# Performance work log

Measured on AMD Instinct MI355X. Metric: run time of the kernel, lower is better.

## Reference

```python
import jax, jax.numpy as jnp
import numpy as np

N_NODES = 10000
N_GRAPHS = 64
IN_DIM = 256
HID = 256
N_CLASSES = 10
N_EDGES = 320000


def _gcn_conv(x, W, b, src, dst):
    # PyG GCNConv: h = x @ W; add self-loops (weight 1); symmetric norm D^-1/2 (A+I) D^-1/2; aggregate; + b
    N = x.shape[0]
    h = x @ W  # [N, H]
    loops = jnp.arange(N, dtype=src.dtype)
    s = jnp.concatenate([src, loops])
    d = jnp.concatenate([dst, loops])
    w = jnp.ones(s.shape[0], dtype=x.dtype)
    deg = jax.ops.segment_sum(w, d, num_segments=N)
    dinv = jnp.where(deg > 0, jax.lax.rsqrt(jnp.maximum(deg, 1.0)), 0.0)
    norm = dinv[s] * dinv[d]  # [E+N]
    msg = h[s] * norm[:, None]  # gather + scale
    out = jax.ops.segment_sum(msg, d, num_segments=N)  # scatter-add
    return out + b


def setup_inputs() -> dict:
    key = jax.random.key(0)
    ks = jax.random.split(key, 12)
    x = jax.random.normal(ks[0], (N_NODES, IN_DIM), dtype=jnp.float32)
    edge_index = jax.random.randint(ks[1], (2, N_EDGES), 0, N_NODES, dtype=jnp.int64)
    batch = jnp.sort(jax.random.randint(ks[2], (N_NODES,), 0, N_GRAPHS, dtype=jnp.int64))
    g = 1.0 / np.sqrt(IN_DIM)
    W1 = jax.random.uniform(ks[3], (IN_DIM, HID), jnp.float32, -g, g)
    b1 = jnp.zeros((HID,), jnp.float32)
    gh = 1.0 / np.sqrt(HID)
    W2 = jax.random.uniform(ks[4], (HID, HID), jnp.float32, -gh, gh)
    b2 = jnp.zeros((HID,), jnp.float32)
    W3 = jax.random.uniform(ks[5], (HID, HID), jnp.float32, -gh, gh)
    b3 = jnp.zeros((HID,), jnp.float32)
    Wlin = jax.random.uniform(ks[6], (HID, N_CLASSES), jnp.float32, -gh, gh)
    blin = jax.random.uniform(ks[7], (N_CLASSES,), jnp.float32, -gh, gh)
    return {"x": x, "W1": W1, "b1": b1, "W2": W2, "b2": b2, "W3": W3, "b3": b3,
            "Wlin": Wlin, "blin": blin, "edge_index": edge_index, "batch": batch}


def reference(x, W1, b1, W2, b2, W3, b3, Wlin, blin, edge_index, batch):
    src, dst = edge_index[0], edge_index[1]
    h = jax.nn.relu(_gcn_conv(x, W1, b1, src, dst))
    h = jax.nn.relu(_gcn_conv(h, W2, b2, src, dst))
    h = jax.nn.relu(_gcn_conv(h, W3, b3, src, dst))
    # global mean pool over graphs (dropout is identity in eval mode)
    sums = jax.ops.segment_sum(h, batch, num_segments=N_GRAPHS)  # [G, H]
    cnts = jax.ops.segment_sum(jnp.ones((h.shape[0],), h.dtype), batch, num_segments=N_GRAPHS)
    pooled = sums / jnp.maximum(cnts, 1.0)[:, None]
    logits = pooled @ Wlin + blin
    return jax.nn.log_softmax(logits, axis=-1)
```

## Files before the change

kernel.cpp:

```cpp
#include <hip/hip_runtime.h>
#include <hip/hip_bf16.h>
#include <math.h>

#define HIDDEN 256
#define NCLS 10

typedef __attribute__((ext_vector_type(8))) short short8;
typedef __attribute__((ext_vector_type(4))) float f32x4;

static __device__ __forceinline__ float bf16lo(unsigned u) {
    return __uint_as_float((u & 0xffffu) << 16);
}
static __device__ __forceinline__ float bf16hi(unsigned u) {
    return __uint_as_float(u & 0xffff0000u);
}
static __device__ __forceinline__ unsigned short f2bf(float f) {
    unsigned x = __float_as_uint(f);
    x += 0x7fffu + ((x >> 16) & 1u);
    return (unsigned short)(x >> 16);
}
static __device__ __forceinline__ unsigned pack2(float lo, float hi) {
    return (unsigned)f2bf(lo) | ((unsigned)f2bf(hi) << 16);
}

static __device__ __forceinline__ void fma8(float* acc, uint4 u, float w) {
    acc[0] = fmaf(bf16lo(u.x), w, acc[0]);
    acc[1] = fmaf(bf16hi(u.x), w, acc[1]);
    acc[2] = fmaf(bf16lo(u.y), w, acc[2]);
    acc[3] = fmaf(bf16hi(u.y), w, acc[3]);
    acc[4] = fmaf(bf16lo(u.z), w, acc[4]);
    acc[5] = fmaf(bf16hi(u.z), w, acc[5]);
    acc[6] = fmaf(bf16lo(u.w), w, acc[6]);
    acc[7] = fmaf(bf16hi(u.w), w, acc[7]);
}

__global__ void k_init(int* ecnt, int* cursor, int N) {
    int i = blockIdx.x * blockDim.x + threadIdx.x;
    if (i < N) { ecnt[i] = 0; cursor[i] = 0; }
}

__global__ void k_count(const int* __restrict__ dst, int* __restrict__ ecnt, int E) {
    int e = blockIdx.x * blockDim.x + threadIdx.x;
    if (e < E) atomicAdd(&ecnt[dst[e]], 1);
}

__global__ void k_dinv(const int* __restrict__ ecnt, float* __restrict__ dinv, int N) {
    int i = blockIdx.x * blockDim.x + threadIdx.x;
    if (i < N) dinv[i] = rsqrtf((float)(ecnt[i] + 1));
}

__global__ void k_scan(const int* __restrict__ ecnt, int* __restrict__ rowstart, int N, int E) {
    __shared__ int sums[1024];
    int t = threadIdx.x;
    const int CH = (N + 1023) / 1024;
    int base = t * CH;
    int local = 0;
    for (int i = 0; i < CH; ++i) {
        int idx = base + i;
        if (idx < N) local += ecnt[idx];
    }
    sums[t] = local;
    __syncthreads();
    for (int off = 1; off < 1024; off <<= 1) {
        int v = (t >= off) ? sums[t - off] : 0;
        __syncthreads();
        sums[t] += v;
        __syncthreads();
    }
    int run = (t == 0) ? 0 : sums[t - 1];
    for (int i = 0; i < CH; ++i) {
        int idx = base + i;
        if (idx < N) { rowstart[idx] = run; run += ecnt[idx]; }
    }
    if (t == 0) rowstart[N] = E;
}

__global__ void k_fill(const int* __restrict__ src, const int* __restrict__ dst,
                       const float* __restrict__ dinv,
                       const int* __restrict__ rowstart, int* __restrict__ cursor,
                       uint2* __restrict__ csr, int E) {
    int e = blockIdx.x * blockDim.x + threadIdx.x;
    if (e < E) {
        int d = dst[e];
        int s = src[e];
        int pos = rowstart[d] + atomicAdd(&cursor[d], 1);
        uint2 ent;
        ent.x = (unsigned)s;
        ent.y = __float_as_uint(dinv[s] * dinv[d]);
        csr[pos] = ent;
    }
}

__global__ void k_cvt(const float* __restrict__ in, unsigned* __restrict__ out, int n4) {
    int i = blockIdx.x * blockDim.x + threadIdx.x;
    if (i < n4) {
        float4 v = reinterpret_cast<const float4*>(in)[i];
        uint2 o;
        o.x = pack2(v.x, v.y);
        o.y = pack2(v.z, v.w);
        reinterpret_cast<uint2*>(out)[i] = o;
    }
}

__global__ void k_packW(const float* __restrict__ W, short8* __restrict__ P) {
    int id = blockIdx.x * blockDim.x + threadIdx.x;
    int l = id & 63;
    int t = (id >> 6) & 15;
    int s = id >> 10;
    int col = t * 16 + (l & 15);
    int k0 = s * 32 + (l >> 4) * 8;
    short8 v;
#pragma unroll
    for (int j = 0; j < 8; ++j)
        v[j] = (short)f2bf(W[(size_t)(k0 + j) * HIDDEN + col]);
    P[id] = v;
}

__global__ __launch_bounds__(256) void k_gemm(const unsigned short* __restrict__ A,
                                              const short8* __restrict__ P,
                                              unsigned short* __restrict__ C) {
    const int l = threadIdx.x & 63;
    const int w = threadIdx.x >> 6;
    const int g = l >> 4;
    const int r = l & 15;
    const int mwave = blockIdx.x * 64 + w * 16;
    const int nb = blockIdx.y * 4;

    f32x4 acc[4] = {f32x4{0,0,0,0}, f32x4{0,0,0,0}, f32x4{0,0,0,0}, f32x4{0,0,0,0}};
    const unsigned short* arow = A + (size_t)(mwave + r) * HIDDEN;

#pragma unroll
    for (int s = 0; s < 8; ++s) {
        short8 a = *reinterpret_cast<const short8*>(arow + s * 32 + g * 8);
#pragma unroll
        for (int f = 0; f < 4; ++f) {
            short8 b = P[(s * 16 + nb + f) * 64 + l];
            acc[f] = __builtin_amdgcn_mfma_f32_16x16x32_bf16(a, b, acc[f], 0, 0, 0);
        }
    }
#pragma unroll
    for (int f = 0; f < 4; ++f) {
        int col = blockIdx.y * 64 + f * 16 + r;
#pragma unroll
        for (int q = 0; q < 4; ++q) {
            int row = mwave + g * 4 + q;
            C[(size_t)row * HIDDEN + col] = f2bf(acc[f][q]);
        }
    }
}

__global__ __launch_bounds__(64) void k_agg(const unsigned* __restrict__ H,
                                            const uint2* __restrict__ csr,
                                            const int* __restrict__ rowstart,
                                            const float* __restrict__ dinv,
                                            const float* __restrict__ bias,
                                            unsigned* __restrict__ out) {
    const int n = blockIdx.x;
    const int l = threadIdx.x;
    const int q = l & 31;
    const int h = l >> 5;
    const uint4* __restrict__ H4 = reinterpret_cast<const uint4*>(H);

    float acc[8] = {0.f, 0.f, 0.f, 0.f, 0.f, 0.f, 0.f, 0.f};
    if (h == 0) {
        const float di = dinv[n];
        fma8(acc, H4[(size_t)n * 32 + q], di * di);
    }

    int e = rowstart[n] + h;
    const int e1 = rowstart[n + 1];
    for (; e + 2 < e1; e += 4) {
        uint2 ed0 = csr[e];
        uint2 ed1 = csr[e + 2];
        uint4 r0 = H4[(size_t)ed0.x * 32 + q];
        uint4 r1 = H4[(size_t)ed1.x * 32 + q];
        fma8(acc, r0, __uint_as_float(ed0.y));
        fma8(acc, r1, __uint_as_float(ed1.y));
    }
    for (; e < e1; e += 2) {
        uint2 ed = csr[e];
        uint4 r0 = H4[(size_t)ed.x * 32 + q];
        fma8(acc, r0, __uint_as_float(ed.y));
    }

#pragma unroll
    for (int j = 0; j < 8; ++j) acc[j] += __shfl_xor(acc[j], 32);

    if (h == 0) {
        const float4* __restrict__ b4 = reinterpret_cast<const float4*>(bias);
        float4 ba = b4[q * 2];
        float4 bb = b4[q * 2 + 1];
        uint4 o;
        o.x = pack2(fmaxf(acc[0] + ba.x, 0.f), fmaxf(acc[1] + ba.y, 0.f));
        o.y = pack2(fmaxf(acc[2] + ba.z, 0.f), fmaxf(acc[3] + ba.w, 0.f));
        o.z = pack2(fmaxf(acc[4] + bb.x, 0.f), fmaxf(acc[5] + bb.y, 0.f));
        o.w = pack2(fmaxf(acc[6] + bb.z, 0.f), fmaxf(acc[7] + bb.w, 0.f));
        reinterpret_cast<uint4*>(out)[(size_t)n * 32 + q] = o;
    }
}

__device__ __forceinline__ int lower_bound_i(const int* a, int n, int val) {
    int lo = 0, hi = n;
    while (lo < hi) {
        int mid = (lo + hi) >> 1;
        if (a[mid] < val) lo = mid + 1; else hi = mid;
    }
    return lo;
}

__global__ __launch_bounds__(128) void k_pool_part(const unsigned* __restrict__ H,
                                                   const int* __restrict__ batch,
                                                   float* __restrict__ partial, int N) {
    const int g = blockIdx.x;
    const int s = blockIdx.y;
    const int p = threadIdx.x;
    const int lo = lower_bound_i(batch, N, g);
    const int hi = lower_bound_i(batch, N, g + 1);
    float sx = 0.f, sy = 0.f;
    for (int n = lo + s; n < hi; n += 8) {
        unsigned u = H[(size_t)n * 128 + p];
        sx += bf16lo(u);
        sy += bf16hi(u);
    }
    float2 v; v.x = sx; v.y = sy;
    reinterpret_cast<float2*>(partial)[(size_t)(g * 8 + s) * 128 + p] = v;
}

__global__ __launch_bounds__(256) void k_cls(const float* __restrict__ partial,
                                             const int* __restrict__ batch,
                                             const float* __restrict__ Wlin,
                                             const float* __restrict__ blin,
                                             float* __restrict__ out, int N) {
    __shared__ float part[NCLS][HIDDEN];
    const int g = blockIdx.x;
    const int t = threadIdx.x;
    const int lo = lower_bound_i(batch, N, g);
    const int hi = lower_bound_i(batch, N, g + 1);
    float p = 0.f;
#pragma unroll
    for (int s = 0; s < 8; ++s) p += partial[(size_t)(g * 8 + s) * HIDDEN + t];
    p /= fmaxf((float)(hi - lo), 1.f);
#pragma unroll
    for (int c = 0; c < NCLS; ++c) part[c][t] = p * Wlin[(size_t)t * NCLS + c];
    __syncthreads();
    for (int off = 128; off >= 1; off >>= 1) {
        if (t < off) {
#pragma unroll
            for (int c = 0; c < NCLS; ++c) part[c][t] += part[c][t + off];
        }
        __syncthreads();
    }
    if (t == 0) {
        float lg[NCLS];
        float m = -INFINITY;
#pragma unroll
        for (int c = 0; c < NCLS; ++c) {
            lg[c] = part[c][0] + blin[c];
            m = fmaxf(m, lg[c]);
        }
        float se = 0.f;
#pragma unroll
        for (int c = 0; c < NCLS; ++c) se += expf(lg[c] - m);
        float lse = m + logf(se);
#pragma unroll
        for (int c = 0; c < NCLS; ++c) out[(size_t)g * NCLS + c] = lg[c] - lse;
    }
}


extern "C" void kernel_launch(void* const* d_in, const int* in_sizes, int n_in,
                              void* d_out, int out_size, void* d_ws, size_t ws_size,
                              hipStream_t stream) {
    const float* x    = (const float*)d_in[0];
    const float* W1   = (const float*)d_in[1];
    const float* b1   = (const float*)d_in[2];
    const float* W2   = (const float*)d_in[3];
    const float* b2   = (const float*)d_in[4];
    const float* W3   = (const float*)d_in[5];
    const float* b3   = (const float*)d_in[6];
    const float* Wlin = (const float*)d_in[7];
    const float* blin = (const float*)d_in[8];
    const int*   eidx = (const int*)d_in[9];
    const int*   batch= (const int*)d_in[10];
    float* out = (float*)d_out;

    const int N = in_sizes[0] / HIDDEN;
    const int E = in_sizes[9] / 2;
    const int G = out_size / NCLS;
    const int Mp = (N + 63) & ~63;

    const int* src = eidx;
    const int* dst = eidx + E;

    char* base = (char*)d_ws;
    size_t off = 0;
    auto alloc = [&](size_t bytes) -> void* {
        void* p = base + off;
        off = (off + bytes + 255) & ~(size_t)255;
        return p;
    };
    int*      ecnt     = (int*)     alloc((size_t)N * sizeof(int));
    int*      cursor   = (int*)     alloc((size_t)N * sizeof(int));
    float*    dinv     = (float*)   alloc((size_t)N * sizeof(float));
    int*      rowstart = (int*)     alloc((size_t)(N + 1) * sizeof(int));
    uint2*    csr      = (uint2*)   alloc((size_t)E * sizeof(uint2));
    unsigned* x16      = (unsigned*)alloc((size_t)Mp * 128 * sizeof(unsigned));
    unsigned* hA       = (unsigned*)alloc((size_t)Mp * 128 * sizeof(unsigned));
    unsigned* hB       = (unsigned*)alloc((size_t)Mp * 128 * sizeof(unsigned));
    short8*   Wp1      = (short8*)  alloc((size_t)8192 * sizeof(short8));
    short8*   Wp2      = (short8*)  alloc((size_t)8192 * sizeof(short8));
    short8*   Wp3      = (short8*)  alloc((size_t)8192 * sizeof(short8));
    float*    partial  = (float*)   alloc((size_t)G * 8 * HIDDEN * sizeof(float));
    (void)ws_size;

    const int T = 256;
    k_init <<<(N + T - 1) / T, T, 0, stream>>>(ecnt, cursor, N);
    k_count<<<(E + T - 1) / T, T, 0, stream>>>(dst, ecnt, E);
    k_dinv <<<(N + T - 1) / T, T, 0, stream>>>(ecnt, dinv, N);
    k_scan <<<1, 1024, 0, stream>>>(ecnt, rowstart, N, E);
    k_fill <<<(E + T - 1) / T, T, 0, stream>>>(src, dst, dinv, rowstart, cursor, csr, E);
    const int n4 = N * HIDDEN / 4;
    k_cvt  <<<(n4 + T - 1) / T, T, 0, stream>>>(x, x16, n4);
    k_packW<<<8192 / T, T, 0, stream>>>(W1, Wp1);
    k_packW<<<8192 / T, T, 0, stream>>>(W2, Wp2);
    k_packW<<<8192 / T, T, 0, stream>>>(W3, Wp3);

    const dim3 ggrid(Mp / 64, 4);
    k_gemm<<<ggrid, T, 0, stream>>>((const unsigned short*)x16, Wp1, (unsigned short*)hA);
    k_agg <<<N, 64, 0, stream>>>(hA, csr, rowstart, dinv, b1, hB);
    k_gemm<<<ggrid, T, 0, stream>>>((const unsigned short*)hB, Wp2, (unsigned short*)hA);
    k_agg <<<N, 64, 0, stream>>>(hA, csr, rowstart, dinv, b2, hB);
    k_gemm<<<ggrid, T, 0, stream>>>((const unsigned short*)hB, Wp3, (unsigned short*)hA);
    k_agg <<<N, 64, 0, stream>>>(hA, csr, rowstart, dinv, b3, hB);
    k_pool_part<<<dim3(G, 8), 128, 0, stream>>>(hB, batch, partial, N);
    k_cls <<<G, T, 0, stream>>>(partial, batch, Wlin, blin, out, N);
}
```

Before: 181.6 us.

## Fuse CSR build into cooperative kernel, merge prep kernels, widen GEMM and agg tiles

The five graph-preprocessing kernels become one cooperative kernel that uses grid syncs and a two-level block scan instead of a single-block scan. The input conversion and the three weight-packing launches are merged into one kernel. The GEMM now computes 128 output columns per block instead of 64, halving grid.y. Aggregation packs four nodes per 256-thread block and unrolls edge gathers by four per half-wave to expose more memory parallelism. All of this targets launch overhead and latency, at the cost of cooperative-launch constraints (512 resident blocks, blocksum sized for 64 scan blocks) and more GEMM registers.

```diff
diff --git a/kernel.cpp b/kernel.cpp
--- a/kernel.cpp
+++ b/kernel.cpp
@@ -1,9 +1,14 @@
 #include <hip/hip_runtime.h>
 #include <hip/hip_bf16.h>
+#include <hip/hip_cooperative_groups.h>
 #include <math.h>
+
+namespace cg = cooperative_groups;
 
 #define HIDDEN 256
 #define NCLS 10
+#define PREB 512
+#define PRET 256
 
 typedef __attribute__((ext_vector_type(8))) short short8;
 typedef __attribute__((ext_vector_type(4))) float f32x4;
@@ -34,56 +39,58 @@
     acc[7] = fmaf(bf16hi(u.w), w, acc[7]);
 }
 
-__global__ void k_init(int* ecnt, int* cursor, int N) {
-    int i = blockIdx.x * blockDim.x + threadIdx.x;
-    if (i < N) { ecnt[i] = 0; cursor[i] = 0; }
-}
-
-__global__ void k_count(const int* __restrict__ dst, int* __restrict__ ecnt, int E) {
-    int e = blockIdx.x * blockDim.x + threadIdx.x;
-    if (e < E) atomicAdd(&ecnt[dst[e]], 1);
-}
-
-__global__ void k_dinv(const int* __restrict__ ecnt, float* __restrict__ dinv, int N) {
-    int i = blockIdx.x * blockDim.x + threadIdx.x;
-    if (i < N) dinv[i] = rsqrtf((float)(ecnt[i] + 1));
-}
-
-__global__ void k_scan(const int* __restrict__ ecnt, int* __restrict__ rowstart, int N, int E) {
-    __shared__ int sums[1024];
-    int t = threadIdx.x;
-    const int CH = (N + 1023) / 1024;
-    int base = t * CH;
-    int local = 0;
-    for (int i = 0; i < CH; ++i) {
-        int idx = base + i;
-        if (idx < N) local += ecnt[idx];
-    }
-    sums[t] = local;
-    __syncthreads();
-    for (int off = 1; off < 1024; off <<= 1) {
-        int v = (t >= off) ? sums[t - off] : 0;
+__global__ __launch_bounds__(PRET) void k_pre(const int* __restrict__ src,
+                                              const int* __restrict__ dst,
+                                              int* __restrict__ ecnt,
+                                              int* __restrict__ rowstart,
+                                              int* __restrict__ cursor,
+                                              float* __restrict__ dinv,
+                                              uint2* __restrict__ csr,
+                                              int* __restrict__ blocksum,
+                                              int N, int E) {
+    cg::grid_group grid = cg::this_grid();
+    const int t = threadIdx.x;
+    const int b = blockIdx.x;
+    const int gtid = b * PRET + t;
+    const int gsz = PREB * PRET;
+
+    for (int i = gtid; i < N; i += gsz) ecnt[i] = 0;
+    grid.sync();
+    for (int e = gtid; e < E; e += gsz) atomicAdd(&ecnt[dst[e]], 1);
+    grid.sync();
+    const int SB = (N + PRET - 1) / PRET;
+    __shared__ int sh[PRET];
+    if (b < SB) {
+        int i = b * PRET + t;
+        int v = (i < N) ? ecnt[i] : 0;
+        sh[t] = v;
         __syncthreads();
-        sums[t] += v;
-        __syncthreads();
-    }
-    int run = (t == 0) ? 0 : sums[t - 1];
-    for (int i = 0; i < CH; ++i) {
-        int idx = base + i;
-        if (idx < N) { rowstart[idx] = run; run += ecnt[idx]; }
-    }
-    if (t == 0) rowstart[N] = E;
-}
-
-__global__ void k_fill(const int* __restrict__ src, const int* __restrict__ dst,
-                       const float* __restrict__ dinv,
-                       const int* __restrict__ rowstart, int* __restrict__ cursor,
-                       uint2* __restrict__ csr, int E) {
-    int e = blockIdx.x * blockDim.x + threadIdx.x;
-    if (e < E) {
-        int d = dst[e];
-        int s = src[e];
-        int pos = rowstart[d] + atomicAdd(&cursor[d], 1);
+        for (int off = 1; off < PRET; off <<= 1) {
+            int add = (t >= off) ? sh[t - off] : 0;
+            __syncthreads();
+            sh[t] += add;
+            __syncthreads();
+        }
+        if (i < N) rowstart[i] = sh[t] - v;
+        if (t == PRET - 1) blocksum[b] = sh[t];
+    }
+    grid.sync();
+    if (b == 0 && t == 0) {
+        int run = 0;
+        for (int i = 0; i < SB; ++i) { int v = blocksum[i]; blocksum[i] = run; run += v; }
+    }
+    grid.sync();
+    for (int i = gtid; i < N; i += gsz) {
+        int rs = rowstart[i] + blocksum[i / PRET];
+        rowstart[i] = rs;
+        cursor[i] = rs;
+        dinv[i] = rsqrtf((float)(ecnt[i] + 1));
+    }
+    if (gtid == 0) rowstart[N] = E;
+    grid.sync();
+    for (int e = gtid; e < E; e += gsz) {
+        int d = dst[e], s = src[e];
+        int pos = atomicAdd(&cursor[d], 1);
         uint2 ent;
         ent.x = (unsigned)s;
         ent.y = __float_as_uint(dinv[s] * dinv[d]);
@@ -91,29 +98,42 @@
     }
 }
 
-__global__ void k_cvt(const float* __restrict__ in, unsigned* __restrict__ out, int n4) {
-    int i = blockIdx.x * blockDim.x + threadIdx.x;
-    if (i < n4) {
-        float4 v = reinterpret_cast<const float4*>(in)[i];
-        uint2 o;
-        o.x = pack2(v.x, v.y);
-        o.y = pack2(v.z, v.w);
-        reinterpret_cast<uint2*>(out)[i] = o;
-    }
-}
-
-__global__ void k_packW(const float* __restrict__ W, short8* __restrict__ P) {
-    int id = blockIdx.x * blockDim.x + threadIdx.x;
-    int l = id & 63;
-    int t = (id >> 6) & 15;
-    int s = id >> 10;
-    int col = t * 16 + (l & 15);
-    int k0 = s * 32 + (l >> 4) * 8;
-    short8 v;
-#pragma unroll
-    for (int j = 0; j < 8; ++j)
-        v[j] = (short)f2bf(W[(size_t)(k0 + j) * HIDDEN + col]);
-    P[id] = v;
+__global__ __launch_bounds__(256) void k_prep(const float* __restrict__ x,
+                                              unsigned* __restrict__ x16,
+                                              const float* __restrict__ W1,
+                                              const float* __restrict__ W2,
+                                              const float* __restrict__ W3,
+                                              short8* __restrict__ P1,
+                                              short8* __restrict__ P2,
+                                              short8* __restrict__ P3,
+                                              int n4, int nb_cvt) {
+    const int b = blockIdx.x;
+    if (b < nb_cvt) {
+        int i = b * 256 + threadIdx.x;
+        if (i < n4) {
+            float4 v = reinterpret_cast<const float4*>(x)[i];
+            uint2 o;
+            o.x = pack2(v.x, v.y);
+            o.y = pack2(v.z, v.w);
+            reinterpret_cast<uint2*>(x16)[i] = o;
+        }
+    } else {
+        int pb = b - nb_cvt;
+        int which = pb >> 5;
+        int id = (pb & 31) * 256 + threadIdx.x;
+        const float* W = (which == 0) ? W1 : (which == 1) ? W2 : W3;
+        short8* P = (which == 0) ? P1 : (which == 1) ? P2 : P3;
+        int l = id & 63;
+        int tt = (id >> 6) & 15;
+        int s = id >> 10;
+        int col = tt * 16 + (l & 15);
+        int k0 = s * 32 + (l >> 4) * 8;
+        short8 v;
+#pragma unroll
+        for (int j = 0; j < 8; ++j)
+            v[j] = (short)f2bf(W[(size_t)(k0 + j) * HIDDEN + col]);
+        P[id] = v;
+    }
 }
 
 __global__ __launch_bounds__(256) void k_gemm(const unsigned short* __restrict__ A,
@@ -124,23 +144,23 @@
     const int g = l >> 4;
     const int r = l & 15;
     const int mwave = blockIdx.x * 64 + w * 16;
-    const int nb = blockIdx.y * 4;
-
-    f32x4 acc[4] = {f32x4{0,0,0,0}, f32x4{0,0,0,0}, f32x4{0,0,0,0}, f32x4{0,0,0,0}};
+    const int nb = blockIdx.y * 8;
+
+    f32x4 acc[8] = {};
     const unsigned short* arow = A + (size_t)(mwave + r) * HIDDEN;
 
 #pragma unroll
     for (int s = 0; s < 8; ++s) {
         short8 a = *reinterpret_cast<const short8*>(arow + s * 32 + g * 8);
 #pragma unroll
-        for (int f = 0; f < 4; ++f) {
-            short8 b = P[(s * 16 + nb + f) * 64 + l];
-            acc[f] = __builtin_amdgcn_mfma_f32_16x16x32_bf16(a, b, acc[f], 0, 0, 0);
-        }
-    }
-#pragma unroll
-    for (int f = 0; f < 4; ++f) {
-        int col = blockIdx.y * 64 + f * 16 + r;
+        for (int f = 0; f < 8; ++f) {
+            short8 bfrag = P[(s * 16 + nb + f) * 64 + l];
+            acc[f] = __builtin_amdgcn_mfma_f32_16x16x32_bf16(a, bfrag, acc[f], 0, 0, 0);
+        }
+    }
+#pragma unroll
+    for (int f = 0; f < 8; ++f) {
+        int col = blockIdx.y * 128 + f * 16 + r;
 #pragma unroll
         for (int q = 0; q < 4; ++q) {
             int row = mwave + g * 4 + q;
@@ -149,14 +169,15 @@
     }
 }
 
-__global__ __launch_bounds__(64) void k_agg(const unsigned* __restrict__ H,
-                                            const uint2* __restrict__ csr,
-                                            const int* __restrict__ rowstart,
-                                            const float* __restrict__ dinv,
-                                            const float* __restrict__ bias,
-                                            unsigned* __restrict__ out) {
-    const int n = blockIdx.x;
-    const int l = threadIdx.x;
+__global__ __launch_bounds__(256) void k_agg(const unsigned* __restrict__ H,
+                                             const uint2* __restrict__ csr,
+                                             const int* __restrict__ rowstart,
+                                             const float* __restrict__ dinv,
+                                             const float* __restrict__ bias,
+                                             unsigned* __restrict__ out, int N) {
+    const int n = blockIdx.x * 4 + (threadIdx.x >> 6);
+    if (n >= N) return;
+    const int l = threadIdx.x & 63;
     const int q = l & 31;
     const int h = l >> 5;
     const uint4* __restrict__ H4 = reinterpret_cast<const uint4*>(H);
@@ -167,18 +188,25 @@
         fma8(acc, H4[(size_t)n * 32 + q], di * di);
     }
 
-    int e = rowstart[n] + h;
+    int e = rowstart[n];
     const int e1 = rowstart[n + 1];
-    for (; e + 2 < e1; e += 4) {
-        uint2 ed0 = csr[e];
-        uint2 ed1 = csr[e + 2];
+    for (; e + 8 <= e1; e += 8) {
+        int bx = e + 4 * h;
+        uint2 ed0 = csr[bx + 0];
+        uint2 ed1 = csr[bx + 1];
+        uint2 ed2 = csr[bx + 2];
+        uint2 ed3 = csr[bx + 3];
         uint4 r0 = H4[(size_t)ed0.x * 32 + q];
         uint4 r1 = H4[(size_t)ed1.x * 32 + q];
+        uint4 r2 = H4[(size_t)ed2.x * 32 + q];
+        uint4 r3 = H4[(size_t)ed3.x * 32 + q];
         fma8(acc, r0, __uint_as_float(ed0.y));
         fma8(acc, r1, __uint_as_float(ed1.y));
-    }
-    for (; e < e1; e += 2) {
-        uint2 ed = csr[e];
+        fma8(acc, r2, __uint_as_float(ed2.y));
+        fma8(acc, r3, __uint_as_float(ed3.y));
+    }
+    for (int te = e + h; te < e1; te += 2) {
+        uint2 ed = csr[te];
         uint4 r0 = H4[(size_t)ed.x * 32 + q];
         fma8(acc, r0, __uint_as_float(ed.y));
     }
@@ -303,6 +331,7 @@
     int*      cursor   = (int*)     alloc((size_t)N * sizeof(int));
     float*    dinv     = (float*)   alloc((size_t)N * sizeof(float));
     int*      rowstart = (int*)     alloc((size_t)(N + 1) * sizeof(int));
+    int*      blocksum = (int*)     alloc((size_t)64 * sizeof(int));
     uint2*    csr      = (uint2*)   alloc((size_t)E * sizeof(uint2));
     unsigned* x16      = (unsigned*)alloc((size_t)Mp * 128 * sizeof(unsigned));
     unsigned* hA       = (unsigned*)alloc((size_t)Mp * 128 * sizeof(unsigned));
@@ -313,25 +342,27 @@
     float*    partial  = (float*)   alloc((size_t)G * 8 * HIDDEN * sizeof(float));
     (void)ws_size;
 
-    const int T = 256;
-    k_init <<<(N + T - 1) / T, T, 0, stream>>>(ecnt, cursor, N);
-    k_count<<<(E + T - 1) / T, T, 0, stream>>>(dst, ecnt, E);
-    k_dinv <<<(N + T - 1) / T, T, 0, stream>>>(ecnt, dinv, N);
-    k_scan <<<1, 1024, 0, stream>>>(ecnt, rowstart, N, E);
-    k_fill <<<(E + T - 1) / T, T, 0, stream>>>(src, dst, dinv, rowstart, cursor, csr, E);
+    {
+        const int* src_ = src; const int* dst_ = dst;
+        int N_ = N, E_ = E;
+        void* args[] = {(void*)&src_, (void*)&dst_, (void*)&ecnt, (void*)&rowstart,
+                        (void*)&cursor, (void*)&dinv, (void*)&csr, (void*)&blocksum,
+                        (void*)&N_, (void*)&E_};
+        hipLaunchCooperativeKernel((void*)k_pre, dim3(PREB), dim3(PRET), args, 0, stream);
+    }
+
     const int n4 = N * HIDDEN / 4;
-    k_cvt  <<<(n4 + T - 1) / T, T, 0, stream>>>(x, x16, n4);
-    k_packW<<<8192 / T, T, 0, stream>>>(W1, Wp1);
-    k_packW<<<8192 / T, T, 0, stream>>>(W2, Wp2);
-    k_packW<<<8192 / T, T, 0, stream>>>(W3, Wp3);
-
-    const dim3 ggrid(Mp / 64, 4);
-    k_gemm<<<ggrid, T, 0, stream>>>((const unsigned short*)x16, Wp1, (unsigned short*)hA);
-    k_agg <<<N, 64, 0, stream>>>(hA, csr, rowstart, dinv, b1, hB);
-    k_gemm<<<ggrid, T, 0, stream>>>((const unsigned short*)hB, Wp2, (unsigned short*)hA);
-    k_agg <<<N, 64, 0, stream>>>(hA, csr, rowstart, dinv, b2, hB);
-    k_gemm<<<ggrid, T, 0, stream>>>((const unsigned short*)hB, Wp3, (unsigned short*)hA);
-    k_agg <<<N, 64, 0, stream>>>(hA, csr, rowstart, dinv, b3, hB);
+    const int nb_cvt = (n4 + 255) / 256;
+    k_prep<<<nb_cvt + 96, 256, 0, stream>>>(x, x16, W1, W2, W3, Wp1, Wp2, Wp3, n4, nb_cvt);
+
+    const dim3 ggrid(Mp / 64, 2);
+    const int agg_blocks = (N + 3) / 4;
+    k_gemm<<<ggrid, 256, 0, stream>>>((const unsigned short*)x16, Wp1, (unsigned short*)hA);
+    k_agg <<<agg_blocks, 256, 0, stream>>>(hA, csr, rowstart, dinv, b1, hB, N);
+    k_gemm<<<ggrid, 256, 0, stream>>>((const unsigned short*)hB, Wp2, (unsigned short*)hA);
+    k_agg <<<agg_blocks, 256, 0, stream>>>(hA, csr, rowstart, dinv, b2, hB, N);
+    k_gemm<<<ggrid, 256, 0, stream>>>((const unsigned short*)hB, Wp3, (unsigned short*)hA);
+    k_agg <<<agg_blocks, 256, 0, stream>>>(hA, csr, rowstart, dinv, b3, hB, N);
     k_pool_part<<<dim3(G, 8), 128, 0, stream>>>(hB, batch, partial, N);
-    k_cls <<<G, T, 0, stream>>>(partial, batch, Wlin, blin, out, N);
-}
+    k_cls <<<G, 256, 0, stream>>>(partial, batch, Wlin, blin, out, N);
+}
```

Measured after the change: 430.7 us. +137.2%, slower.
